# Performance work log

Measured on AMD Instinct MI355X. Metric: run time of the kernel, lower is better.

Reference implementation:

```python
import math
import jax, jax.numpy as jnp
import numpy as np

B, N, K, E, NUM_EDGES, T_STEPS = 2, 512, 128, 768, 1536, 1010
PI = 3.14159  # matches the torch.jit.script gaussian constant


def timestep_embedding(t, dim):
    # standard sinusoidal ("positional") diffusion timestep embedding
    half = dim // 2
    freqs = jnp.exp(-math.log(10000.0) * jnp.arange(half, dtype=jnp.float32) / half)
    args = t.astype(jnp.float32)[:, None] * freqs  # [B, half]
    return jnp.concatenate([jnp.cos(args), jnp.sin(args)], axis=-1)  # [B, K]


def setup_inputs() -> dict:
    key = jax.random.key(0)
    ks = jax.random.split(key, 16)
    inp = {
        "pos": jax.random.normal(ks[0], (B, N, 3), dtype=jnp.float32) * 3.0,
        "node_type_edge": jax.random.randint(ks[1], (B, N, N, 2), 0, NUM_EDGES),
        "padding_mask": jax.random.randint(ks[2], (B, N), 0, 2).astype(bool),
        "mask_aa": jax.random.randint(ks[3], (B, N, 1), 0, 2).astype(bool),
        "mask_pos": jax.random.randint(ks[4], (B, N, 1), 0, 2).astype(bool),
        "time_pos": jax.random.randint(ks[5], (B,), 0, T_STEPS),
        # GaussianLayer params
        "means": jax.random.uniform(ks[6], (1, K), minval=0.0, maxval=3.0),
        "stds": jax.random.uniform(ks[7], (1, K), minval=0.0, maxval=3.0),
        "mul_w": 1.0 + 0.1 * jax.random.normal(ks[8], (NUM_EDGES, 1)),
        "bias_w": 0.1 * jax.random.normal(ks[9], (NUM_EDGES, 1)),
        # edge_proj Linear(K, E)
        "proj_w": jax.random.normal(ks[10], (K, E)) / math.sqrt(K),
        "proj_b": jnp.zeros((E,), jnp.float32),
        # TimeStepEncoder MLP (Linear K->K, SiLU, Linear K->K)
        "t_w1": jax.random.normal(ks[11], (K, K)) / math.sqrt(K),
        "t_b1": jnp.zeros((K,), jnp.float32),
        "t_w2": jax.random.normal(ks[12], (K, K)) / math.sqrt(K),
        "t_b2": jnp.zeros((K,), jnp.float32),
    }
    return inp


def reference(pos, node_type_edge, padding_mask, mask_aa, mask_pos, time_pos,
              means, stds, mul_w, bias_w, proj_w, proj_b, t_w1, t_b1, t_w2, t_b2):
    # pairwise displacements / distances: delta_pos[b,i,j] = pos[b,j] - pos[b,i]
    delta_pos = pos[:, None, :, :] - pos[:, :, None, :]            # [B,N,N,3]
    dist = jnp.linalg.norm(delta_pos, axis=-1)                     # [B,N,N]
    delta_pos = delta_pos / (dist[..., None] + 1e-5)

    # mask edge types where either endpoint amino acid is masked
    node_mask_i = jnp.broadcast_to(mask_aa[:, :, None, :], (B, N, N, 1))
    node_mask_j = jnp.broadcast_to(mask_aa[:, None, :, :], (B, N, N, 1))
    new_node_mask = jnp.concatenate([node_mask_i, node_mask_j], axis=-1)  # [B,N,N,2]
    nte = jnp.where(new_node_mask, 0, node_type_edge)

    # GaussianLayer
    mul = mul_w[nte].sum(axis=-2)                                  # [B,N,N,1]
    bias = bias_w[nte].sum(axis=-2)                                # [B,N,N,1]
    x = mul * dist[..., None] + bias                               # [B,N,N,1]
    mean = means.reshape(-1)                                       # [K]
    std = jnp.abs(stds.reshape(-1)) + 0.01                         # [K]
    a = (2.0 * PI) ** 0.5
    edge_feature = jnp.exp(-0.5 * ((x - mean) / std) ** 2) / (a * std)  # [B,N,N,K]

    # time embedding (t.repeat_i + t.repeat_j == 2*t broadcast over i,j)
    def t_enc(t):
        e = timestep_embedding(t, K)
        h = jax.nn.silu(e @ t_w1 + t_b1)
        return h @ t_w2 + t_b2                                     # [B,K]

    t = t_enc(time_pos)[:, None, None, :]                          # [B,1,1,K]
    t0 = t_enc(jnp.zeros_like(time_pos))[:, None, None, :]         # [B,1,1,K]
    mask_dist = mask_pos[:, :, None, :] | mask_pos[:, None, :, :]  # [B,N,N,1]
    edge_feature = edge_feature + jnp.where(mask_dist, 2.0 * t, 2.0 * t0)

    # zero out padded j-nodes, reduce over j, project
    edge_feature = jnp.where(padding_mask[:, None, :, None], 0.0, edge_feature)
    sum_edge_features = edge_feature.sum(axis=-2)                  # [B,N,K]
    merge = sum_edge_features @ proj_w + proj_b                    # [B,N,E]
    merge = jnp.where(padding_mask[..., None], 0.0, merge)
    return edge_feature, merge, delta_pos
```

## Files before the change

kernel.cpp:

```cpp
#include <hip/hip_runtime.h>
#include <hip/hip_bf16.h>
#include <math.h>

#define BB 2
#define NN 512
#define KK 128
#define EE 768
#define NUM_EDGES 1536

__global__ __launch_bounds__(256) void edge_fused_kernel(
    const float* __restrict__ pos,
    const int* __restrict__ node_type_edge,
    const int* __restrict__ padding_mask,
    const int* __restrict__ mask_aa,
    const int* __restrict__ mask_pos,
    const int* __restrict__ time_pos,
    const float* __restrict__ means,
    const float* __restrict__ stds,
    const float* __restrict__ mul_w,
    const float* __restrict__ bias_w,
    const float* __restrict__ proj_w,
    const float* __restrict__ proj_b,
    const float* __restrict__ t_w1, const float* __restrict__ t_b1,
    const float* __restrict__ t_w2, const float* __restrict__ t_b2,
    float* __restrict__ out_ef,
    float* __restrict__ out_merge,
    float* __restrict__ out_dp)
{
    __shared__ float e2[2][KK];
    __shared__ float h2[2][KK];
    __shared__ float tv[2][KK];
    __shared__ float xv[NN];
    __shared__ unsigned char fl[NN];
    __shared__ float red[4 * KK];

    const int bi = blockIdx.x;
    const int b = bi >> 9;
    const int i = bi & (NN - 1);
    const int tid = threadIdx.x;

    {
        const int enc = tid >> 7;
        const int k = tid & 127;
        const float t = (enc == 0) ? (float)time_pos[b] : 0.0f;
        const int kk = k & 63;
        const float freq = __expf(-logf(10000.0f) * (float)kk * (1.0f / 64.0f));
        const float arg = t * freq;
        e2[enc][k] = (k < 64) ? cosf(arg) : sinf(arg);
        __syncthreads();

        float acc = t_b1[k];
#pragma unroll 8
        for (int r = 0; r < KK; ++r) acc += e2[enc][r] * t_w1[r * KK + k];
        h2[enc][k] = acc / (1.0f + __expf(-acc));
        __syncthreads();

        float acc2 = t_b2[k];
#pragma unroll 8
        for (int r = 0; r < KK; ++r) acc2 += h2[enc][r] * t_w2[r * KK + k];
        tv[enc][k] = 2.0f * acc2;
    }

    const float pix = pos[(b * NN + i) * 3 + 0];
    const float piy = pos[(b * NN + i) * 3 + 1];
    const float piz = pos[(b * NN + i) * 3 + 2];
    const int maa_i  = mask_aa[b * NN + i];
    const int mpos_i = mask_pos[b * NN + i];

    for (int j = tid; j < NN; j += 256) {
        const float dx = pos[(b * NN + j) * 3 + 0] - pix;
        const float dy = pos[(b * NN + j) * 3 + 1] - piy;
        const float dz = pos[(b * NN + j) * 3 + 2] - piz;
        const float dist = sqrtf(dx * dx + dy * dy + dz * dz);
        const float invd = 1.0f / (dist + 1e-5f);
        const size_t dpo = ((size_t)bi * NN + j) * 3;
        out_dp[dpo + 0] = dx * invd;
        out_dp[dpo + 1] = dy * invd;
        out_dp[dpo + 2] = dz * invd;

        const int base = (bi * NN + j) * 2;
        int e0 = node_type_edge[base + 0];
        int e1 = node_type_edge[base + 1];
        if (maa_i)               e0 = 0;
        if (mask_aa[b * NN + j]) e1 = 0;
        const float mul  = mul_w[e0]  + mul_w[e1];
        const float bias = bias_w[e0] + bias_w[e1];
        xv[j] = mul * dist + bias;

        const int md  = (mpos_i | mask_pos[b * NN + j]) ? 1 : 0;
        const int pad = padding_mask[b * NN + j] ? 2 : 0;
        fl[j] = (unsigned char)(md | pad);
    }
    __syncthreads();

    const int k0 = (tid & 63) * 2;
    const int jg = tid >> 6;
    const float a = sqrtf(2.0f * 3.14159f);

    const float mean0 = means[k0];
    const float mean1 = means[k0 + 1];
    const float sd0 = fabsf(stds[k0]) + 0.01f;
    const float sd1 = fabsf(stds[k0 + 1]) + 0.01f;
    const float inv0 = 1.0f / sd0, inv1 = 1.0f / sd1;
    const float coef0 = 1.0f / (a * sd0), coef1 = 1.0f / (a * sd1);
    const float t2_0  = tv[0][k0];
    const float t2_1  = tv[0][k0 + 1];
    const float t02_0 = tv[1][k0];
    const float t02_1 = tv[1][k0 + 1];

    float s0 = 0.0f, s1 = 0.0f;
    const size_t efbase = (size_t)bi * NN * KK;

    for (int jj = 0; jj < NN / 4; ++jj) {
        const int j = jj * 4 + jg;
        const float x = xv[j];
        const unsigned char f = fl[j];

        const float u0 = (x - mean0) * inv0;
        const float u1 = (x - mean1) * inv1;
        float v0 = __expf(-0.5f * u0 * u0) * coef0 + ((f & 1) ? t2_0 : t02_0);
        float v1 = __expf(-0.5f * u1 * u1) * coef1 + ((f & 1) ? t2_1 : t02_1);
        if (f & 2) { v0 = 0.0f; v1 = 0.0f; }
        s0 += v0; s1 += v1;

        float2 pack; pack.x = v0; pack.y = v1;
        *reinterpret_cast<float2*>(&out_ef[efbase + (size_t)j * KK + k0]) = pack;
    }

    red[jg * KK + k0]     = s0;
    red[jg * KK + k0 + 1] = s1;
    __syncthreads();

    if (tid < KK) {
        const int k = tid;
        red[k] = red[k] + red[KK + k] + red[2 * KK + k] + red[3 * KK + k];
    }
    __syncthreads();

    const bool pad_i = padding_mask[b * NN + i] != 0;
#pragma unroll
    for (int r = 0; r < 3; ++r) {
        const int e = tid + r * 256;
        float acc = proj_b[e];
#pragma unroll 16
        for (int k = 0; k < KK; ++k)
            acc += red[k] * proj_w[k * EE + e];
        out_merge[(size_t)bi * EE + e] = pad_i ? 0.0f : acc;
    }
}

extern "C" void kernel_launch(void* const* d_in, const int* in_sizes, int n_in,
                              void* d_out, int out_size, void* d_ws, size_t ws_size,
                              hipStream_t stream) {
    const float* pos          = (const float*)d_in[0];
    const int* node_type_edge = (const int*)d_in[1];
    const int* padding_mask   = (const int*)d_in[2];
    const int* mask_aa        = (const int*)d_in[3];
    const int* mask_pos       = (const int*)d_in[4];
    const int* time_pos       = (const int*)d_in[5];
    const float* means        = (const float*)d_in[6];
    const float* stds         = (const float*)d_in[7];
    const float* mul_w        = (const float*)d_in[8];
    const float* bias_w       = (const float*)d_in[9];
    const float* proj_w       = (const float*)d_in[10];
    const float* proj_b       = (const float*)d_in[11];
    const float* t_w1         = (const float*)d_in[12];
    const float* t_b1         = (const float*)d_in[13];
    const float* t_w2         = (const float*)d_in[14];
    const float* t_b2         = (const float*)d_in[15];

    float* out       = (float*)d_out;
    float* out_ef    = out;
    float* out_merge = out + (size_t)BB * NN * NN * KK;
    float* out_dp    = out_merge + (size_t)BB * NN * EE;

    edge_fused_kernel<<<BB * NN, 256, 0, stream>>>(
        pos, node_type_edge, padding_mask, mask_aa, mask_pos, time_pos,
        means, stds, mul_w, bias_w, proj_w, proj_b,
        t_w1, t_b1, t_w2, t_b2,
        out_ef, out_merge, out_dp);
}
```

Measured before the change: 63.48 us.

## Split fused kernel into time-encoder, edge, and tiled projection kernels

Before, every one of the 1024 blocks recomputed the two-layer time MLP and ran its own 128x768 projection GEMV. Now a tiny kernel computes the time embeddings once into workspace. The main edge kernel writes per-row sums to workspace and uses float4 stores. A separate tiled kernel then does the projection for 8 rows per block, so each proj_w load is reused 8 times. This adds two kernel launches and a workspace round-trip, and falls back to the old fused kernel if the workspace is too small.

After: 73.86 us. +16.3%, slower.

```diff
diff --git a/kernel.cpp b/kernel.cpp
--- a/kernel.cpp
+++ b/kernel.cpp
@@ -7,6 +7,193 @@
 #define KK 128
 #define EE 768
 #define NUM_EDGES 1536
+#define MR 8
+
+#define WS_SUMS_OFF 384
+#define WS_REQ_BYTES ((size_t)(WS_SUMS_OFF + BB * NN * KK) * 4)
+
+__global__ __launch_bounds__(128) void tenc_kernel(
+    const int* __restrict__ time_pos,
+    const float* __restrict__ t_w1, const float* __restrict__ t_b1,
+    const float* __restrict__ t_w2, const float* __restrict__ t_b2,
+    float* __restrict__ ws)
+{
+    __shared__ float e[KK];
+    __shared__ float h[KK];
+    const int enc = blockIdx.x;
+    const int k = threadIdx.x;
+    const float t = (enc < BB) ? (float)time_pos[enc] : 0.0f;
+
+    {
+        const int kk = k & 63;
+        const float freq = __expf(-logf(10000.0f) * (float)kk * (1.0f / 64.0f));
+        const float arg = t * freq;
+        e[k] = (k < 64) ? cosf(arg) : sinf(arg);
+    }
+    __syncthreads();
+
+    float acc = t_b1[k];
+#pragma unroll 8
+    for (int r = 0; r < KK; ++r) acc += e[r] * t_w1[r * KK + k];
+    h[k] = acc / (1.0f + __expf(-acc));
+    __syncthreads();
+
+    float acc2 = t_b2[k];
+#pragma unroll 8
+    for (int r = 0; r < KK; ++r) acc2 += h[r] * t_w2[r * KK + k];
+
+    ws[enc * KK + k] = 2.0f * acc2;
+}
+
+__global__ __launch_bounds__(256) void edge_main_kernel(
+    const float* __restrict__ pos,
+    const int* __restrict__ node_type_edge,
+    const int* __restrict__ padding_mask,
+    const int* __restrict__ mask_aa,
+    const int* __restrict__ mask_pos,
+    const float* __restrict__ means,
+    const float* __restrict__ stds,
+    const float* __restrict__ mul_w,
+    const float* __restrict__ bias_w,
+    const float* __restrict__ ws_t,
+    float* __restrict__ ws_sums,
+    float* __restrict__ out_ef,
+    float* __restrict__ out_dp)
+{
+    __shared__ float xv[NN];
+    __shared__ unsigned char fl[NN];
+    __shared__ float red[8 * KK];
+
+    const int bi = blockIdx.x;
+    const int b = bi >> 9;
+    const int i = bi & (NN - 1);
+    const int tid = threadIdx.x;
+
+    const float pix = pos[(b * NN + i) * 3 + 0];
+    const float piy = pos[(b * NN + i) * 3 + 1];
+    const float piz = pos[(b * NN + i) * 3 + 2];
+    const int maa_i  = mask_aa[b * NN + i];
+    const int mpos_i = mask_pos[b * NN + i];
+
+    for (int j = tid; j < NN; j += 256) {
+        const float dx = pos[(b * NN + j) * 3 + 0] - pix;
+        const float dy = pos[(b * NN + j) * 3 + 1] - piy;
+        const float dz = pos[(b * NN + j) * 3 + 2] - piz;
+        const float dist = sqrtf(dx * dx + dy * dy + dz * dz);
+        const float invd = 1.0f / (dist + 1e-5f);
+        const size_t dpo = ((size_t)bi * NN + j) * 3;
+        out_dp[dpo + 0] = dx * invd;
+        out_dp[dpo + 1] = dy * invd;
+        out_dp[dpo + 2] = dz * invd;
+
+        const int base = (bi * NN + j) * 2;
+        int e0 = node_type_edge[base + 0];
+        int e1 = node_type_edge[base + 1];
+        if (maa_i)               e0 = 0;
+        if (mask_aa[b * NN + j]) e1 = 0;
+        const float mul  = mul_w[e0]  + mul_w[e1];
+        const float bias = bias_w[e0] + bias_w[e1];
+        xv[j] = mul * dist + bias;
+
+        const int md  = (mpos_i | mask_pos[b * NN + j]) ? 1 : 0;
+        const int pad = padding_mask[b * NN + j] ? 2 : 0;
+        fl[j] = (unsigned char)(md | pad);
+    }
+    __syncthreads();
+
+    const int k0 = (tid & 31) * 4;
+    const int jg = tid >> 5;
+    const float a = sqrtf(2.0f * 3.14159f);
+
+    float mean[4], inv[4], coef[4], t2[4], t02[4];
+#pragma unroll
+    for (int q = 0; q < 4; ++q) {
+        mean[q] = means[k0 + q];
+        const float sd = fabsf(stds[k0 + q]) + 0.01f;
+        inv[q]  = 1.0f / sd;
+        coef[q] = 1.0f / (a * sd);
+        t2[q]   = ws_t[b * KK + k0 + q];
+        t02[q]  = ws_t[2 * KK + k0 + q];
+    }
+
+    float s[4] = {0.0f, 0.0f, 0.0f, 0.0f};
+    const size_t efbase = (size_t)bi * NN * KK;
+
+    for (int jj = 0; jj < NN / 8; ++jj) {
+        const int j = jj * 8 + jg;
+        const float x = xv[j];
+        const unsigned char f = fl[j];
+        float v[4];
+#pragma unroll
+        for (int q = 0; q < 4; ++q) {
+            const float u = (x - mean[q]) * inv[q];
+            float val = __expf(-0.5f * u * u) * coef[q] + ((f & 1) ? t2[q] : t02[q]);
+            if (f & 2) val = 0.0f;
+            s[q] += val;
+            v[q] = val;
+        }
+        float4 st; st.x = v[0]; st.y = v[1]; st.z = v[2]; st.w = v[3];
+        *reinterpret_cast<float4*>(&out_ef[efbase + (size_t)j * KK + k0]) = st;
+    }
+
+#pragma unroll
+    for (int q = 0; q < 4; ++q) red[jg * KK + k0 + q] = s[q];
+    __syncthreads();
+
+    if (tid < KK) {
+        float t = 0.0f;
+#pragma unroll
+        for (int g = 0; g < 8; ++g) t += red[g * KK + tid];
+        ws_sums[(size_t)bi * KK + tid] = t;
+    }
+}
+
+__global__ __launch_bounds__(256) void merge_tiled_kernel(
+    const float* __restrict__ ws_sums,
+    const float* __restrict__ proj_w,
+    const float* __restrict__ proj_b,
+    const int* __restrict__ padding_mask,
+    float* __restrict__ out_merge)
+{
+    __shared__ float s[MR][KK];
+    __shared__ int pad[MR];
+    const int row0 = blockIdx.x * MR;
+    const int tid = threadIdx.x;
+
+    for (int idx = tid; idx < MR * KK; idx += 256)
+        s[idx >> 7][idx & 127] = ws_sums[(size_t)row0 * KK + idx];
+    if (tid < MR) pad[tid] = padding_mask[row0 + tid];
+    __syncthreads();
+
+    const int e0 = tid, e1 = tid + 256, e2 = tid + 512;
+    float acc0[MR], acc1[MR], acc2[MR];
+#pragma unroll
+    for (int m = 0; m < MR; ++m) { acc0[m] = 0.0f; acc1[m] = 0.0f; acc2[m] = 0.0f; }
+
+#pragma unroll 4
+    for (int k = 0; k < KK; ++k) {
+        const float w0 = proj_w[k * EE + e0];
+        const float w1 = proj_w[k * EE + e1];
+        const float w2 = proj_w[k * EE + e2];
+#pragma unroll
+        for (int m = 0; m < MR; ++m) {
+            const float sv = s[m][k];
+            acc0[m] += sv * w0;
+            acc1[m] += sv * w1;
+            acc2[m] += sv * w2;
+        }
+    }
+
+    const float pb0 = proj_b[e0], pb1 = proj_b[e1], pb2 = proj_b[e2];
+#pragma unroll
+    for (int m = 0; m < MR; ++m) {
+        const size_t o = (size_t)(row0 + m) * EE;
+        const bool p = pad[m] != 0;
+        out_merge[o + e0] = p ? 0.0f : (acc0[m] + pb0);
+        out_merge[o + e1] = p ? 0.0f : (acc1[m] + pb1);
+        out_merge[o + e2] = p ? 0.0f : (acc2[m] + pb2);
+    }
+}
 
 __global__ __launch_bounds__(256) void edge_fused_kernel(
     const float* __restrict__ pos,
@@ -173,10 +360,20 @@
     float* out_ef    = out;
     float* out_merge = out + (size_t)BB * NN * NN * KK;
     float* out_dp    = out_merge + (size_t)BB * NN * EE;
-
-    edge_fused_kernel<<<BB * NN, 256, 0, stream>>>(
-        pos, node_type_edge, padding_mask, mask_aa, mask_pos, time_pos,
-        means, stds, mul_w, bias_w, proj_w, proj_b,
-        t_w1, t_b1, t_w2, t_b2,
-        out_ef, out_merge, out_dp);
-}
+    float* ws        = (float*)d_ws;
+
+    if (ws_size >= WS_REQ_BYTES) {
+        tenc_kernel<<<3, 128, 0, stream>>>(time_pos, t_w1, t_b1, t_w2, t_b2, ws);
+        edge_main_kernel<<<BB * NN, 256, 0, stream>>>(
+            pos, node_type_edge, padding_mask, mask_aa, mask_pos,
+            means, stds, mul_w, bias_w, ws, ws + WS_SUMS_OFF, out_ef, out_dp);
+        merge_tiled_kernel<<<(BB * NN) / MR, 256, 0, stream>>>(
+            ws + WS_SUMS_OFF, proj_w, proj_b, padding_mask, out_merge);
+    } else {
+        edge_fused_kernel<<<BB * NN, 256, 0, stream>>>(
+            pos, node_type_edge, padding_mask, mask_aa, mask_pos, time_pos,
+            means, stds, mul_w, bias_w, proj_w, proj_b,
+            t_w1, t_b1, t_w2, t_b2,
+            out_ef, out_merge, out_dp);
+    }
+}
```

## Process four rows per block to amortize time-MLP and reuse proj_w across rows

Applied to the files above, without the earlier changes.

Each block now handles four (b,i) rows instead of one. The per-block timestep-embedding MLP is computed once for four rows, and the final projection loads each proj_w element once and applies it to all four row sums. The grid shrinks from 1024 to 256 blocks, which on a GPU with many CUs lowers parallelism for the store-bound edge_feature write, and the row loop serializes the distance and Gaussian phases within a block.

After: 70.11 us. 1.1x slower.

```diff
diff --git a/kernel.cpp b/kernel.cpp
--- a/kernel.cpp
+++ b/kernel.cpp
@@ -7,8 +7,9 @@
 #define KK 128
 #define EE 768
 #define NUM_EDGES 1536
-
-__global__ __launch_bounds__(256) void edge_fused_kernel(
+#define ROWS 4
+
+__global__ __launch_bounds__(256) void edge_persist_kernel(
     const float* __restrict__ pos,
     const int* __restrict__ node_type_edge,
     const int* __restrict__ padding_mask,
@@ -33,10 +34,11 @@
     __shared__ float xv[NN];
     __shared__ unsigned char fl[NN];
     __shared__ float red[4 * KK];
-
-    const int bi = blockIdx.x;
-    const int b = bi >> 9;
-    const int i = bi & (NN - 1);
+    __shared__ float sums[ROWS][KK];
+    __shared__ int   padr[ROWS];
+
+    const int bi0 = blockIdx.x * ROWS;
+    const int b = bi0 >> 9;
     const int tid = threadIdx.x;
 
     {
@@ -61,91 +63,113 @@
         tv[enc][k] = 2.0f * acc2;
     }
 
-    const float pix = pos[(b * NN + i) * 3 + 0];
-    const float piy = pos[(b * NN + i) * 3 + 1];
-    const float piz = pos[(b * NN + i) * 3 + 2];
-    const int maa_i  = mask_aa[b * NN + i];
-    const int mpos_i = mask_pos[b * NN + i];
-
-    for (int j = tid; j < NN; j += 256) {
-        const float dx = pos[(b * NN + j) * 3 + 0] - pix;
-        const float dy = pos[(b * NN + j) * 3 + 1] - piy;
-        const float dz = pos[(b * NN + j) * 3 + 2] - piz;
-        const float dist = sqrtf(dx * dx + dy * dy + dz * dz);
-        const float invd = 1.0f / (dist + 1e-5f);
-        const size_t dpo = ((size_t)bi * NN + j) * 3;
-        out_dp[dpo + 0] = dx * invd;
-        out_dp[dpo + 1] = dy * invd;
-        out_dp[dpo + 2] = dz * invd;
-
-        const int base = (bi * NN + j) * 2;
-        int e0 = node_type_edge[base + 0];
-        int e1 = node_type_edge[base + 1];
-        if (maa_i)               e0 = 0;
-        if (mask_aa[b * NN + j]) e1 = 0;
-        const float mul  = mul_w[e0]  + mul_w[e1];
-        const float bias = bias_w[e0] + bias_w[e1];
-        xv[j] = mul * dist + bias;
-
-        const int md  = (mpos_i | mask_pos[b * NN + j]) ? 1 : 0;
-        const int pad = padding_mask[b * NN + j] ? 2 : 0;
-        fl[j] = (unsigned char)(md | pad);
-    }
-    __syncthreads();
-
     const int k0 = (tid & 63) * 2;
     const int jg = tid >> 6;
     const float a = sqrtf(2.0f * 3.14159f);
-
     const float mean0 = means[k0];
     const float mean1 = means[k0 + 1];
     const float sd0 = fabsf(stds[k0]) + 0.01f;
     const float sd1 = fabsf(stds[k0 + 1]) + 0.01f;
     const float inv0 = 1.0f / sd0, inv1 = 1.0f / sd1;
     const float coef0 = 1.0f / (a * sd0), coef1 = 1.0f / (a * sd1);
+    __syncthreads();
     const float t2_0  = tv[0][k0];
     const float t2_1  = tv[0][k0 + 1];
     const float t02_0 = tv[1][k0];
     const float t02_1 = tv[1][k0 + 1];
 
-    float s0 = 0.0f, s1 = 0.0f;
-    const size_t efbase = (size_t)bi * NN * KK;
-
-    for (int jj = 0; jj < NN / 4; ++jj) {
-        const int j = jj * 4 + jg;
-        const float x = xv[j];
-        const unsigned char f = fl[j];
-
-        const float u0 = (x - mean0) * inv0;
-        const float u1 = (x - mean1) * inv1;
-        float v0 = __expf(-0.5f * u0 * u0) * coef0 + ((f & 1) ? t2_0 : t02_0);
-        float v1 = __expf(-0.5f * u1 * u1) * coef1 + ((f & 1) ? t2_1 : t02_1);
-        if (f & 2) { v0 = 0.0f; v1 = 0.0f; }
-        s0 += v0; s1 += v1;
-
-        float2 pack; pack.x = v0; pack.y = v1;
-        *reinterpret_cast<float2*>(&out_ef[efbase + (size_t)j * KK + k0]) = pack;
-    }
-
-    red[jg * KK + k0]     = s0;
-    red[jg * KK + k0 + 1] = s1;
-    __syncthreads();
-
-    if (tid < KK) {
-        const int k = tid;
-        red[k] = red[k] + red[KK + k] + red[2 * KK + k] + red[3 * KK + k];
-    }
-    __syncthreads();
-
-    const bool pad_i = padding_mask[b * NN + i] != 0;
+    for (int r = 0; r < ROWS; ++r) {
+        const int bi = bi0 + r;
+        const int i = bi & (NN - 1);
+
+        const float pix = pos[(b * NN + i) * 3 + 0];
+        const float piy = pos[(b * NN + i) * 3 + 1];
+        const float piz = pos[(b * NN + i) * 3 + 2];
+        const int maa_i  = mask_aa[b * NN + i];
+        const int mpos_i = mask_pos[b * NN + i];
+
+        for (int j = tid; j < NN; j += 256) {
+            const float dx = pos[(b * NN + j) * 3 + 0] - pix;
+            const float dy = pos[(b * NN + j) * 3 + 1] - piy;
+            const float dz = pos[(b * NN + j) * 3 + 2] - piz;
+            const float dist = sqrtf(dx * dx + dy * dy + dz * dz);
+            const float invd = 1.0f / (dist + 1e-5f);
+            const size_t dpo = ((size_t)bi * NN + j) * 3;
+            out_dp[dpo + 0] = dx * invd;
+            out_dp[dpo + 1] = dy * invd;
+            out_dp[dpo + 2] = dz * invd;
+
+            const int base = (bi * NN + j) * 2;
+            int e0 = node_type_edge[base + 0];
+            int e1 = node_type_edge[base + 1];
+            if (maa_i)               e0 = 0;
+            if (mask_aa[b * NN + j]) e1 = 0;
+            const float mul  = mul_w[e0]  + mul_w[e1];
+            const float bias = bias_w[e0] + bias_w[e1];
+            xv[j] = mul * dist + bias;
+
+            const int md  = (mpos_i | mask_pos[b * NN + j]) ? 1 : 0;
+            const int pad = padding_mask[b * NN + j] ? 2 : 0;
+            fl[j] = (unsigned char)(md | pad);
+        }
+        if (tid == 0) padr[r] = padding_mask[b * NN + i];
+        __syncthreads();
+
+        float s0 = 0.0f, s1 = 0.0f;
+        const size_t efbase = (size_t)bi * NN * KK;
+
+#pragma unroll 8
+        for (int jj = 0; jj < NN / 4; ++jj) {
+            const int j = jj * 4 + jg;
+            const float x = xv[j];
+            const unsigned char f = fl[j];
+
+            const float u0 = (x - mean0) * inv0;
+            const float u1 = (x - mean1) * inv1;
+            float v0 = __expf(-0.5f * u0 * u0) * coef0 + ((f & 1) ? t2_0 : t02_0);
+            float v1 = __expf(-0.5f * u1 * u1) * coef1 + ((f & 1) ? t2_1 : t02_1);
+            if (f & 2) { v0 = 0.0f; v1 = 0.0f; }
+            s0 += v0; s1 += v1;
+
+            float2 pack; pack.x = v0; pack.y = v1;
+            *reinterpret_cast<float2*>(&out_ef[efbase + (size_t)j * KK + k0]) = pack;
+        }
+
+        red[jg * KK + k0]     = s0;
+        red[jg * KK + k0 + 1] = s1;
+        __syncthreads();
+
+        if (tid < KK)
+            sums[r][tid] = red[tid] + red[KK + tid] + red[2 * KK + tid] + red[3 * KK + tid];
+        __syncthreads();
+    }
+
+    float acc0[ROWS], acc1[ROWS], acc2[ROWS];
 #pragma unroll
-    for (int r = 0; r < 3; ++r) {
-        const int e = tid + r * 256;
-        float acc = proj_b[e];
-#pragma unroll 16
-        for (int k = 0; k < KK; ++k)
-            acc += red[k] * proj_w[k * EE + e];
-        out_merge[(size_t)bi * EE + e] = pad_i ? 0.0f : acc;
+    for (int r = 0; r < ROWS; ++r) { acc0[r] = 0.0f; acc1[r] = 0.0f; acc2[r] = 0.0f; }
+
+#pragma unroll 4
+    for (int k = 0; k < KK; ++k) {
+        const float w0 = proj_w[k * EE + tid];
+        const float w1 = proj_w[k * EE + tid + 256];
+        const float w2 = proj_w[k * EE + tid + 512];
+#pragma unroll
+        for (int r = 0; r < ROWS; ++r) {
+            const float sv = sums[r][k];
+            acc0[r] += sv * w0;
+            acc1[r] += sv * w1;
+            acc2[r] += sv * w2;
+        }
+    }
+
+    const float pb0 = proj_b[tid], pb1 = proj_b[tid + 256], pb2 = proj_b[tid + 512];
+#pragma unroll
+    for (int r = 0; r < ROWS; ++r) {
+        const size_t o = (size_t)(bi0 + r) * EE;
+        const bool p = padr[r] != 0;
+        out_merge[o + tid]       = p ? 0.0f : (acc0[r] + pb0);
+        out_merge[o + tid + 256] = p ? 0.0f : (acc1[r] + pb1);
+        out_merge[o + tid + 512] = p ? 0.0f : (acc2[r] + pb2);
     }
 }
 
@@ -174,7 +198,7 @@
     float* out_merge = out + (size_t)BB * NN * NN * KK;
     float* out_dp    = out_merge + (size_t)BB * NN * EE;
 
-    edge_fused_kernel<<<BB * NN, 256, 0, stream>>>(
+    edge_persist_kernel<<<(BB * NN) / ROWS, 256, 0, stream>>>(
         pos, node_type_edge, padding_mask, mask_aa, mask_pos, time_pos,
         means, stds, mul_w, bias_w, proj_w, proj_b,
         t_w1, t_b1, t_w2, t_b2,
```

## Process four rows per block to amortize time MLP and share projection weights

Applied to the files above, without the earlier changes.

Each block now handles four (b,i) rows with 1024 threads instead of one row with 256 threads. The time-embedding MLP is computed once per four rows instead of once per row. Each proj_w load is reused across four accumulators in the final projection. The trade-off is a quarter as many blocks, larger blocks, more shared memory per block, and idle threads during the serial MLP phase and the 768-thread projection phase.

After: 59.78 us. 5.8% less time.

```diff
diff --git a/kernel.cpp b/kernel.cpp
--- a/kernel.cpp
+++ b/kernel.cpp
@@ -7,8 +7,9 @@
 #define KK 128
 #define EE 768
 #define NUM_EDGES 1536
-
-__global__ __launch_bounds__(256) void edge_fused_kernel(
+#define RPB 4
+
+__global__ __launch_bounds__(1024) void edge_fused4_kernel(
     const float* __restrict__ pos,
     const int* __restrict__ node_type_edge,
     const int* __restrict__ padding_mask,
@@ -30,31 +31,42 @@
     __shared__ float e2[2][KK];
     __shared__ float h2[2][KK];
     __shared__ float tv[2][KK];
-    __shared__ float xv[NN];
-    __shared__ unsigned char fl[NN];
-    __shared__ float red[4 * KK];
-
-    const int bi = blockIdx.x;
-    const int b = bi >> 9;
-    const int i = bi & (NN - 1);
+    __shared__ float xv[RPB][NN];
+    __shared__ unsigned char fl[RPB][NN];
+    __shared__ float red[RPB][4 * KK];
+    __shared__ float sums[RPB][KK];
+    __shared__ int padr[RPB];
+
+    const int bi0 = blockIdx.x * RPB;
+    const int b = bi0 >> 9;
     const int tid = threadIdx.x;
-
-    {
-        const int enc = tid >> 7;
-        const int k = tid & 127;
+    const int grp = tid >> 8;
+    const int gt  = tid & 255;
+    const int bi  = bi0 + grp;
+    const int i   = bi & (NN - 1);
+
+    if (grp == 0) {
+        const int enc = gt >> 7;
+        const int k = gt & 127;
         const float t = (enc == 0) ? (float)time_pos[b] : 0.0f;
         const int kk = k & 63;
         const float freq = __expf(-logf(10000.0f) * (float)kk * (1.0f / 64.0f));
         const float arg = t * freq;
         e2[enc][k] = (k < 64) ? cosf(arg) : sinf(arg);
-        __syncthreads();
-
+    }
+    __syncthreads();
+    if (grp == 0) {
+        const int enc = gt >> 7;
+        const int k = gt & 127;
         float acc = t_b1[k];
 #pragma unroll 8
         for (int r = 0; r < KK; ++r) acc += e2[enc][r] * t_w1[r * KK + k];
         h2[enc][k] = acc / (1.0f + __expf(-acc));
-        __syncthreads();
-
+    }
+    __syncthreads();
+    if (grp == 0) {
+        const int enc = gt >> 7;
+        const int k = gt & 127;
         float acc2 = t_b2[k];
 #pragma unroll 8
         for (int r = 0; r < KK; ++r) acc2 += h2[enc][r] * t_w2[r * KK + k];
@@ -67,7 +79,7 @@
     const int maa_i  = mask_aa[b * NN + i];
     const int mpos_i = mask_pos[b * NN + i];
 
-    for (int j = tid; j < NN; j += 256) {
+    for (int j = gt; j < NN; j += 256) {
         const float dx = pos[(b * NN + j) * 3 + 0] - pix;
         const float dy = pos[(b * NN + j) * 3 + 1] - piy;
         const float dz = pos[(b * NN + j) * 3 + 2] - piz;
@@ -85,16 +97,17 @@
         if (mask_aa[b * NN + j]) e1 = 0;
         const float mul  = mul_w[e0]  + mul_w[e1];
         const float bias = bias_w[e0] + bias_w[e1];
-        xv[j] = mul * dist + bias;
+        xv[grp][j] = mul * dist + bias;
 
         const int md  = (mpos_i | mask_pos[b * NN + j]) ? 1 : 0;
         const int pad = padding_mask[b * NN + j] ? 2 : 0;
-        fl[j] = (unsigned char)(md | pad);
-    }
-    __syncthreads();
-
-    const int k0 = (tid & 63) * 2;
-    const int jg = tid >> 6;
+        fl[grp][j] = (unsigned char)(md | pad);
+    }
+    if (gt == 0) padr[grp] = padding_mask[b * NN + i];
+    __syncthreads();
+
+    const int k0 = (gt & 63) * 2;
+    const int jg = gt >> 6;
     const float a = sqrtf(2.0f * 3.14159f);
 
     const float mean0 = means[k0];
@@ -110,11 +123,13 @@
 
     float s0 = 0.0f, s1 = 0.0f;
     const size_t efbase = (size_t)bi * NN * KK;
+    const float* __restrict__ xvr = xv[grp];
+    const unsigned char* __restrict__ flr = fl[grp];
 
     for (int jj = 0; jj < NN / 4; ++jj) {
         const int j = jj * 4 + jg;
-        const float x = xv[j];
-        const unsigned char f = fl[j];
+        const float x = xvr[j];
+        const unsigned char f = flr[j];
 
         const float u0 = (x - mean0) * inv0;
         const float u1 = (x - mean1) * inv1;
@@ -127,25 +142,35 @@
         *reinterpret_cast<float2*>(&out_ef[efbase + (size_t)j * KK + k0]) = pack;
     }
 
-    red[jg * KK + k0]     = s0;
-    red[jg * KK + k0 + 1] = s1;
-    __syncthreads();
-
-    if (tid < KK) {
-        const int k = tid;
-        red[k] = red[k] + red[KK + k] + red[2 * KK + k] + red[3 * KK + k];
-    }
-    __syncthreads();
-
-    const bool pad_i = padding_mask[b * NN + i] != 0;
-#pragma unroll
-    for (int r = 0; r < 3; ++r) {
-        const int e = tid + r * 256;
-        float acc = proj_b[e];
-#pragma unroll 16
-        for (int k = 0; k < KK; ++k)
-            acc += red[k] * proj_w[k * EE + e];
-        out_merge[(size_t)bi * EE + e] = pad_i ? 0.0f : acc;
+    red[grp][jg * KK + k0]     = s0;
+    red[grp][jg * KK + k0 + 1] = s1;
+    __syncthreads();
+
+    if (tid < RPB * KK) {
+        const int r = tid >> 7;
+        const int k = tid & 127;
+        const float* rr = red[r];
+        sums[r][k] = rr[k] + rr[KK + k] + rr[2 * KK + k] + rr[3 * KK + k];
+    }
+    __syncthreads();
+
+    if (tid < EE) {
+        const int e = tid;
+        float acc0 = 0.f, acc1 = 0.f, acc2 = 0.f, acc3 = 0.f;
+#pragma unroll 8
+        for (int k = 0; k < KK; ++k) {
+            const float w = proj_w[k * EE + e];
+            acc0 += sums[0][k] * w;
+            acc1 += sums[1][k] * w;
+            acc2 += sums[2][k] * w;
+            acc3 += sums[3][k] * w;
+        }
+        const float pb = proj_b[e];
+        const size_t o = (size_t)bi0 * EE;
+        out_merge[o + e]          = padr[0] ? 0.0f : (acc0 + pb);
+        out_merge[o + EE + e]     = padr[1] ? 0.0f : (acc1 + pb);
+        out_merge[o + 2 * EE + e] = padr[2] ? 0.0f : (acc2 + pb);
+        out_merge[o + 3 * EE + e] = padr[3] ? 0.0f : (acc3 + pb);
     }
 }
 
@@ -174,7 +199,7 @@
     float* out_merge = out + (size_t)BB * NN * NN * KK;
     float* out_dp    = out_merge + (size_t)BB * NN * EE;
 
-    edge_fused_kernel<<<BB * NN, 256, 0, stream>>>(
+    edge_fused4_kernel<<<(BB * NN) / RPB, 1024, 0, stream>>>(
         pos, node_type_edge, padding_mask, mask_aa, mask_pos, time_pos,
         means, stds, mul_w, bias_w, proj_w, proj_b,
         t_w1, t_b1, t_w2, t_b2,
```
